# Performance work log

Measured on AMD Instinct MI355X. Metric: run time of the kernel, lower is better.

## Reference

```python
import jax, jax.numpy as jnp
import numpy as np

HID = 64  # GRU hidden size fixed in source: layers.GRU(64, ...)


def setup_inputs() -> dict:
    key = jax.random.key(0)
    ks = jax.random.split(key, 9)
    B, T, D, K = 128, 1024, 128, 32
    s = 0.05
    X = jax.random.normal(ks[0], (B, T, D), jnp.float32)
    mask = jnp.ones((B, T), jnp.int32)  # 1 = valid token
    # Keras GRU (reset_after=True) params
    gru_kernel = jax.random.normal(ks[1], (D, 3 * HID), jnp.float32) * s
    gru_rec_kernel = jax.random.normal(ks[2], (HID, 3 * HID), jnp.float32) * s
    gru_bias = jax.random.normal(ks[3], (2, 3 * HID), jnp.float32) * s  # [input_bias, recurrent_bias]
    # tfa.layers.CRF params: dense projection + chain kernel + boundary energies
    dense_kernel = jax.random.normal(ks[4], (HID, K), jnp.float32) * s
    dense_bias = jax.random.normal(ks[5], (K,), jnp.float32) * s
    chain_kernel = jax.random.normal(ks[6], (K, K), jnp.float32) * s
    left_boundary = jax.random.normal(ks[7], (K,), jnp.float32) * s
    right_boundary = jax.random.normal(ks[8], (K,), jnp.float32) * s
    return {"X": X, "mask": mask, "gru_kernel": gru_kernel,
            "gru_rec_kernel": gru_rec_kernel, "gru_bias": gru_bias,
            "dense_kernel": dense_kernel, "dense_bias": dense_bias,
            "chain_kernel": chain_kernel, "left_boundary": left_boundary,
            "right_boundary": right_boundary}


def gru_forward(X, mask_bool, gru_kernel, gru_rec_kernel, gru_bias):
    # Keras GRU, reset_after=True: z/r/h gate ordering, tanh/sigmoid activations.
    B, T, D = X.shape
    xproj = X @ gru_kernel + gru_bias[0]  # [B,T,3H] input projection (fused GEMM)

    def step(h, inp):
        xp, mt = inp  # xp: [B,3H], mt: [B] bool
        rec = h @ gru_rec_kernel + gru_bias[1]  # [B,3H]
        xz, xr, xh = jnp.split(xp, 3, axis=-1)
        rz, rr, rh = jnp.split(rec, 3, axis=-1)
        z = jax.nn.sigmoid(xz + rz)
        r = jax.nn.sigmoid(xr + rr)
        hh = jnp.tanh(xh + r * rh)
        hn = z * h + (1.0 - z) * hh
        hn = jnp.where(mt[:, None], hn, h)  # masked steps carry state
        return hn, hn

    h0 = jnp.zeros((B, HID), X.dtype)
    _, hs = jax.lax.scan(step, h0, (jnp.swapaxes(xproj, 0, 1), jnp.swapaxes(mask_bool, 0, 1)))
    return jnp.swapaxes(hs, 0, 1)  # [B,T,H]


def viterbi_decode(potentials, chain_kernel):
    # Max-plus DP with backpointers; potentials: [B,T,K]
    pots = jnp.swapaxes(potentials, 0, 1)  # [T,B,K]

    def fwd(score, pot_t):
        s = score[:, :, None] + chain_kernel[None]  # [B,K_from,K_to]
        bp = jnp.argmax(s, axis=1).astype(jnp.int32)  # [B,K]
        new_score = jnp.max(s, axis=1) + pot_t
        return new_score, bp

    final_score, bps = jax.lax.scan(fwd, pots[0], pots[1:])  # bps: [T-1,B,K]
    last_tag = jnp.argmax(final_score, axis=-1).astype(jnp.int32)  # [B]

    def back(tag, bp):
        prev = jnp.take_along_axis(bp, tag[:, None], axis=1)[:, 0]
        return prev, tag

    first_tag, tags = jax.lax.scan(back, last_tag, bps, reverse=True)  # tags[t] = tag at step t+1
    decoded = jnp.concatenate([first_tag[None], tags], axis=0)  # [T,B]
    return jnp.swapaxes(decoded, 0, 1)  # [B,T]


def reference(X, mask, gru_kernel, gru_rec_kernel, gru_bias,
              dense_kernel, dense_bias, chain_kernel,
              left_boundary, right_boundary):
    B, T, D = X.shape
    mask_bool = mask == 1
    hidden = gru_forward(X, mask_bool, gru_kernel, gru_rec_kernel, gru_bias)
    potentials = hidden @ dense_kernel + dense_bias  # [B,T,K] emissions
    seq_len = jnp.sum(mask, axis=1).astype(jnp.int32)  # [B]
    # Boundary energies (tfa CRF use_boundary=True): left at t=0, right at last valid step
    potentials = potentials.at[:, 0].add(left_boundary)
    potentials = potentials.at[jnp.arange(B), seq_len - 1].add(right_boundary)
    decoded = viterbi_decode(potentials, chain_kernel)  # [B,T] int32
    return decoded, potentials, seq_len, chain_kernel
```

## Files before the change

kernel.cpp:

```cpp
#include <hip/hip_runtime.h>
#include <math.h>

#define BB 128
#define TT 1024
#define DD 128
#define HH 64
#define G3 192
#define KK 32
#define CH 32

#define BCAST(v, l) __int_as_float(__builtin_amdgcn_readlane(__float_as_int(v), (l)))

__device__ int g_pflags[BB * 32];

__global__ __launch_bounds__(256, 2) void xproj_kernel(const float* __restrict__ X,
                                                       const float* __restrict__ Wk,
                                                       const float* __restrict__ gbias,
                                                       float* __restrict__ xp) {
    __shared__ float Xs[64 * 132];
    __shared__ float Ws[128 * 68];
    const int tid = threadIdx.x;
    const int row0 = blockIdx.x * 64;
    const int cg = blockIdx.y;
#pragma unroll
    for (int it = 0; it < 8; ++it) {
        int idx = it * 1024 + tid * 4;
        int r = idx >> 7, c = idx & 127;
        float4 v = *(const float4*)&X[((size_t)(row0 + r)) * DD + c];
        *(float4*)&Xs[r * 132 + c] = v;
    }
#pragma unroll
    for (int it = 0; it < 8; ++it) {
        int idx = it * 1024 + tid * 4;
        int k = idx >> 6, c = idx & 63;
        float4 v = *(const float4*)&Wk[(size_t)k * G3 + cg * 64 + c];
        *(float4*)&Ws[k * 68 + c] = v;
    }
    __syncthreads();
    const int tr = tid >> 4, tc = tid & 15;
    const int r0 = tr * 4, c0 = tc * 4;
    float acc[4][4];
#pragma unroll
    for (int r = 0; r < 4; ++r)
#pragma unroll
        for (int c = 0; c < 4; ++c) acc[r][c] = 0.f;
#pragma unroll 4
    for (int k = 0; k < DD; k += 4) {
        float a[4][4];
#pragma unroll
        for (int r = 0; r < 4; ++r) {
            float4 t = *(const float4*)&Xs[(r0 + r) * 132 + k];
            a[r][0] = t.x; a[r][1] = t.y; a[r][2] = t.z; a[r][3] = t.w;
        }
#pragma unroll
        for (int kk = 0; kk < 4; ++kk) {
            float4 b = *(const float4*)&Ws[(k + kk) * 68 + c0];
#pragma unroll
            for (int r = 0; r < 4; ++r) {
                acc[r][0] += a[r][kk] * b.x;
                acc[r][1] += a[r][kk] * b.y;
                acc[r][2] += a[r][kk] * b.z;
                acc[r][3] += a[r][kk] * b.w;
            }
        }
    }
    float4 bias = *(const float4*)&gbias[cg * 64 + c0];
#pragma unroll
    for (int r = 0; r < 4; ++r) {
        float4 o;
        o.x = acc[r][0] + bias.x; o.y = acc[r][1] + bias.y;
        o.z = acc[r][2] + bias.z; o.w = acc[r][3] + bias.w;
        *(float4*)&xp[((size_t)(row0 + r0 + r)) * G3 + cg * 64 + c0] = o;
    }
}

__global__ __launch_bounds__(256, 1)
void gruvit_kernel(const float* __restrict__ xp,
                   const float* __restrict__ Wr,
                   const float* __restrict__ gbias,
                   const int* __restrict__ mask,
                   const float* __restrict__ Dk,
                   const float* __restrict__ db,
                   const float* __restrict__ chain,
                   const float* __restrict__ lb,
                   const float* __restrict__ rb,
                   float* __restrict__ out_pot,
                   float* __restrict__ out_dec,
                   float* __restrict__ out_slen,
                   float* __restrict__ out_chn) {
    __shared__ __align__(16) unsigned char smem[73856];
    const int tid = threadIdx.x;
    const int w = tid >> 6;
    const int l = tid & 63;

    if (blockIdx.x < BB) {
        const int b = blockIdx.x;
        const int bTT = b * TT;
        float (*gbuf)[4 * HH]     = (float (*)[4 * HH])(smem);
        float (*hbuf)[HH]         = (float (*)[HH])(smem + 2048);
        float (*potring)[KK]      = (float (*)[KK])(smem + 3072);
        float (*xpstage)[CH * G3] = (float (*)[CH * G3])(smem + 11264);
        int (*maskst)[CH]         = (int (*)[CH])(smem + 60416);

        if (w < 3) {
            const int j = l;
            float wg[HH];
#pragma unroll
            for (int i2 = 0; i2 < HH; ++i2) wg[i2] = Wr[i2 * G3 + w * HH + j];
#pragma unroll
            for (int i2 = 0; i2 < HH; ++i2) asm volatile("" : "+v"(wg[i2]));
            const float bw = gbias[G3 + w * HH + j];
            __builtin_amdgcn_s_setprio(1);
            float h = 0.f;
            __syncthreads();
            float xv0 = xpstage[0][tid];
            int m0 = maskst[0][0];
            for (int i = 0; i < TT + 2; ++i) {
                if (i < TT) {
                    float a0 = bw, a1 = 0.f, a2 = 0.f, a3 = 0.f;
#pragma unroll
                    for (int c = 0; c < HH; c += 4) {
                        a0 += BCAST(h, c + 0) * wg[c + 0];
                        a1 += BCAST(h, c + 1) * wg[c + 1];
                        a2 += BCAST(h, c + 2) * wg[c + 2];
                        a3 += BCAST(h, c + 3) * wg[c + 3];
                    }
                    float a = (a0 + a1) + (a2 + a3);
                    float g = (w == 2) ? a : 1.f / (1.f + __expf(-(xv0 + a)));
                    gbuf[i & 1][w * HH + j] = g;
                    if (w == 2) gbuf[i & 1][3 * HH + j] = xv0;
                }
                __syncthreads();
                if (i < TT) {
                    float z  = gbuf[i & 1][j];
                    float r  = gbuf[i & 1][HH + j];
                    float rh = gbuf[i & 1][2 * HH + j];
                    float xh = gbuf[i & 1][3 * HH + j];
                    float y = xh + r * rh;
                    float hh = 1.f - 2.f / (1.f + __expf(2.f * y));
                    float hn = z * h + (1.f - z) * hh;
                    hn = (m0 != 0) ? hn : h;
                    h = hn;
                    if (w == 0) hbuf[i & 3][j] = hn;
                    if (i < TT - 1) {
                        const int t1 = i + 1;
                        xv0 = xpstage[(t1 >> 5) & 1][(t1 & 31) * G3 + tid];
                        m0  = maskst[(t1 >> 5) & 1][t1 & 31];
                    }
                }
            }
        } else {
            const int k = l & 31;
            int sl = 0;
#pragma unroll
            for (int q = 0; q < 16; ++q) sl += mask[bTT + q * 64 + l];
#pragma unroll
            for (int d = 32; d >= 1; d >>= 1) sl += __shfl_xor(sl, d, 64);
            if (l == 0) out_slen[b] = (float)sl;
            float dk[HH];
#pragma unroll
            for (int i2 = 0; i2 < HH; ++i2) dk[i2] = Dk[i2 * KK + k];
#pragma unroll
            for (int i2 = 0; i2 < HH; ++i2) asm volatile("" : "+v"(dk[i2]));
            const float dbk = db[k], lbk = lb[k], rbk = rb[k];
            const float* xpg = xp + (size_t)bTT * G3;
            float* potg = out_pot + (size_t)bTT * KK;
#pragma unroll
            for (int q = 0; q < 24; ++q) {
                float4 v = *(const float4*)&xpg[q * 256 + l * 4];
                *(float4*)&xpstage[0][q * 256 + l * 4] = v;
            }
            if (l < CH) maskst[0][l] = mask[bTT + l];
            __syncthreads();
            for (int i = 0; i < TT + 2; ++i) {
                if ((i & 31) == 0) {
                    const int cn = (i >> 5) + 1;
                    if (cn < 32) {
                        const float* src = xpg + (size_t)cn * CH * G3;
                        float* dst = &xpstage[cn & 1][0];
#pragma unroll
                        for (int q = 0; q < 24; ++q) {
                            float4 v = *(const float4*)&src[q * 256 + l * 4];
                            *(float4*)&dst[q * 256 + l * 4] = v;
                        }
                        if (l < CH) maskst[cn & 1][l] = mask[bTT + cn * CH + l];
                    }
                    const int cf = (i >> 5) - 2;
                    if (cf >= 0) {
                        const float* srcl = &potring[(cf & 1) * 32][0];
                        float* dstg = potg + (size_t)cf * CH * KK;
#pragma unroll
                        for (int q = 0; q < 4; ++q) {
                            float4 v = *(const float4*)&srcl[q * 256 + l * 4];
                            *(float4*)&dstg[q * 256 + l * 4] = v;
                        }
                    }
                }
                if ((i & 31) == 4 && l == 0) {
                    const int cp = (i >> 5) - 2;
                    if (cp >= 0) {
                        __threadfence();
                        atomicExch(&g_pflags[b * 32 + cp], 1);
                    }
                }
                const int t = i - 2;
                if (t >= 0 && t < TT) {
                    const float4* hv4 = (const float4*)&hbuf[t & 3][0];
                    float p0 = dbk, p1 = 0.f, p2 = 0.f, p3 = 0.f;
#pragma unroll
                    for (int c = 0; c < 16; ++c) {
                        float4 hv = hv4[c];
                        p0 += hv.x * dk[4 * c + 0];
                        p1 += hv.y * dk[4 * c + 1];
                        p2 += hv.z * dk[4 * c + 2];
                        p3 += hv.w * dk[4 * c + 3];
                    }
                    float pot = (p0 + p1) + (p2 + p3);
                    if (t == 0) pot += lbk;
                    if (t == sl - 1) pot += rbk;
                    if (l < 32) potring[t & 63][k] = pot;
                }
                __syncthreads();
            }
            {
                const float* srcl = &potring[(31 & 1) * 32][0];
                float* dstg = potg + (size_t)31 * CH * KK;
#pragma unroll
                for (int q = 0; q < 4; ++q) {
                    float4 v = *(const float4*)&srcl[q * 256 + l * 4];
                    *(float4*)&dstg[q * 256 + l * 4] = v;
                }
                if (l == 0) {
                    __threadfence();
                    atomicExch(&g_pflags[b * 32 + 30], 1);
                    atomicExch(&g_pflags[b * 32 + 31], 1);
                }
            }
        }
        return;
    }

    const int b = blockIdx.x - BB;
    const int bTT = b * TT;
    const float* potg = out_pot + (size_t)bTT * KK;
    const int k = l & 31;
    const int hf = l >> 5;
    const int addrx = (l ^ 32) * 4;

    unsigned char* bp    = smem;
    unsigned char* table = smem + 32736;
    float (*potbuf)[CH][KK] = (float (*)[CH][KK])(smem + 65504);
    int* ent        = (int*)(smem + 73696);
    int* last_tag_s = (int*)(smem + 73824);

    float ccol[16];
    int addr[16];
    if (w == 1) {
#pragma unroll
        for (int m = 0; m < 16; ++m) {
            ccol[m] = chain[(hf * 16 + m) * KK + k];
            addr[m] = (hf * 16 + m) * 4;
        }
#pragma unroll
        for (int m = 0; m < 16; ++m) asm volatile("" : "+v"(ccol[m]));
    }
    if (w == 0) {
        if (l == 0) {
            while (atomicAdd(&g_pflags[b * 32 + 0], 0) == 0) __builtin_amdgcn_s_sleep(8);
        }
        __threadfence();
#pragma unroll
        for (int q = 0; q < 4; ++q) {
            float4 v = *(const float4*)&potg[(size_t)(q * 64 + l) * 4];
            ((float4*)&potbuf[0][0][0])[q * 64 + l] = v;
        }
    }
    __syncthreads();
    float s = 0.f;
    for (int c = 0; c < 32; ++c) {
        if (w == 0 && c + 1 < 32) {
            if (l == 0) {
                while (atomicAdd(&g_pflags[b * 32 + c + 1], 0) == 0)
                    __builtin_amdgcn_s_sleep(8);
            }
            __threadfence();
            const float* src = potg + (size_t)(c + 1) * CH * KK;
#pragma unroll
            for (int q = 0; q < 4; ++q) {
                float4 v = *(const float4*)&src[(size_t)(q * 64 + l) * 4];
                ((float4*)&potbuf[(c + 1) & 1][0][0])[q * 64 + l] = v;
            }
        }
        if (w == 1) {
            for (int ll = 0; ll < 32; ++ll) {
                const int t = c * 32 + ll;
                float pot = potbuf[c & 1][ll][k];
                if (t == 0) {
                    s = pot;
                } else {
                    const int si = __float_as_int(s);
                    float cc[16];
#pragma unroll
                    for (int m = 0; m < 16; ++m)
                        cc[m] = __int_as_float(__builtin_amdgcn_ds_bpermute(addr[m], si)) + ccol[m];
                    float v1[8]; int i1[8];
#pragma unroll
                    for (int p = 0; p < 8; ++p) {
                        bool tk = cc[2 * p + 1] > cc[2 * p];
                        v1[p] = tk ? cc[2 * p + 1] : cc[2 * p];
                        i1[p] = hf * 16 + (tk ? 2 * p + 1 : 2 * p);
                    }
                    float v2[4]; int i2[4];
#pragma unroll
                    for (int p = 0; p < 4; ++p) {
                        bool tk = v1[2 * p + 1] > v1[2 * p];
                        v2[p] = tk ? v1[2 * p + 1] : v1[2 * p];
                        i2[p] = tk ? i1[2 * p + 1] : i1[2 * p];
                    }
                    float v3[2]; int i3[2];
#pragma unroll
                    for (int p = 0; p < 2; ++p) {
                        bool tk = v2[2 * p + 1] > v2[2 * p];
                        v3[p] = tk ? v2[2 * p + 1] : v2[2 * p];
                        i3[p] = tk ? i2[2 * p + 1] : i2[2 * p];
                    }
                    bool tk = v3[1] > v3[0];
                    float bv = tk ? v3[1] : v3[0];
                    int bi = tk ? i3[1] : i3[0];
                    float ov = __int_as_float(__builtin_amdgcn_ds_bpermute(addrx, __float_as_int(bv)));
                    int   oi = __builtin_amdgcn_ds_bpermute(addrx, bi);
                    bool take = (ov > bv) || (ov == bv && oi < bi);
                    if (take) { bv = ov; bi = oi; }
                    if (l < 32) bp[(t - 1) * KK + k] = (unsigned char)bi;
                    s = bv + pot;
                }
            }
        }
        __syncthreads();
    }
    if (w == 1) {
        float bv = s; int bi = k;
#pragma unroll
        for (int d = 16; d >= 1; d >>= 1) {
            float ov = __shfl_xor(bv, d, 64);
            int   oi = __shfl_xor(bi, d, 64);
            bool take = (ov > bv) || (ov == bv && oi < bi);
            if (take) { bv = ov; bi = oi; }
        }
        if (l == 0) *last_tag_s = bi;
    }
    __syncthreads();
    {
        const int kk2 = tid & 31;
        const int grp = tid >> 5;
        for (int c = grp; c < 32; c += 8) {
            int tag = kk2;
            for (int ll = 31; ll >= 0; --ll) {
                const int t = c * 32 + ll;
                if (t < TT - 1) tag = bp[t * KK + tag];
                table[(c * 32 + ll) * KK + kk2] = (unsigned char)tag;
            }
        }
    }
    __syncthreads();
    if (tid == 0) {
        int e = *last_tag_s;
        ent[31] = e;
        for (int c = 30; c >= 0; --c) { e = table[(c + 1) * 32 * KK + e]; ent[c] = e; }
    }
    __syncthreads();
    for (int t = tid; t < TT; t += 256) {
        const int c = t >> 5, ll = t & 31;
        out_dec[(size_t)bTT + t] = (float)table[(c * 32 + ll) * KK + ent[c]];
    }
    if (blockIdx.x == BB) {
        for (int i2 = tid; i2 < KK * KK; i2 += 256) out_chn[i2] = chain[i2];
    }
    for (int i2 = tid; i2 < 32; i2 += 256) atomicExch(&g_pflags[b * 32 + i2], 0);
}

extern "C" void kernel_launch(void* const* d_in, const int* in_sizes, int n_in,
                              void* d_out, int out_size, void* d_ws, size_t ws_size,
                              hipStream_t stream) {
    const float* X     = (const float*)d_in[0];
    const int*   mask  = (const int*)d_in[1];
    const float* Wk    = (const float*)d_in[2];
    const float* Wr    = (const float*)d_in[3];
    const float* gb    = (const float*)d_in[4];
    const float* Dk    = (const float*)d_in[5];
    const float* db    = (const float*)d_in[6];
    const float* chain = (const float*)d_in[7];
    const float* lb    = (const float*)d_in[8];
    const float* rb    = (const float*)d_in[9];

    float* out = (float*)d_out;
    float* out_dec  = out;
    float* out_pot  = out + (size_t)BB * TT;
    float* out_slen = out + (size_t)BB * TT + (size_t)BB * TT * KK;
    float* out_chn  = out_slen + BB;

    float* xp = (float*)d_ws;

    xproj_kernel<<<dim3((BB * TT) / 64, 3), dim3(256), 0, stream>>>(X, Wk, gb, xp);
    gruvit_kernel<<<dim3(2 * BB), dim3(256), 0, stream>>>(xp, Wr, gb, mask, Dk, db,
                                                          chain, lb, rb, out_pot,
                                                          out_dec, out_slen, out_chn);
}
```

Baseline: 745.9 us.

## Fuse GRU input projection GEMM into the per-batch recurrent kernel prologue

Removes the separate xproj kernel launch. Each of the 128 recurrent blocks now computes its own sequence's input projection in a prologue, holding the whole input weight matrix in enlarged shared memory, before the serial GRU scan starts. This saves a launch and the global-wide GEMM phase. In exchange the GEMM runs on only 128 blocks instead of thousands, adds a serial prologue before each recurrence, and raises shared memory use, which limits occupancy.

```diff
diff --git a/kernel.cpp b/kernel.cpp
--- a/kernel.cpp
+++ b/kernel.cpp
@@ -13,69 +13,10 @@
 
 __device__ int g_pflags[BB * 32];
 
-__global__ __launch_bounds__(256, 2) void xproj_kernel(const float* __restrict__ X,
-                                                       const float* __restrict__ Wk,
-                                                       const float* __restrict__ gbias,
-                                                       float* __restrict__ xp) {
-    __shared__ float Xs[64 * 132];
-    __shared__ float Ws[128 * 68];
-    const int tid = threadIdx.x;
-    const int row0 = blockIdx.x * 64;
-    const int cg = blockIdx.y;
-#pragma unroll
-    for (int it = 0; it < 8; ++it) {
-        int idx = it * 1024 + tid * 4;
-        int r = idx >> 7, c = idx & 127;
-        float4 v = *(const float4*)&X[((size_t)(row0 + r)) * DD + c];
-        *(float4*)&Xs[r * 132 + c] = v;
-    }
-#pragma unroll
-    for (int it = 0; it < 8; ++it) {
-        int idx = it * 1024 + tid * 4;
-        int k = idx >> 6, c = idx & 63;
-        float4 v = *(const float4*)&Wk[(size_t)k * G3 + cg * 64 + c];
-        *(float4*)&Ws[k * 68 + c] = v;
-    }
-    __syncthreads();
-    const int tr = tid >> 4, tc = tid & 15;
-    const int r0 = tr * 4, c0 = tc * 4;
-    float acc[4][4];
-#pragma unroll
-    for (int r = 0; r < 4; ++r)
-#pragma unroll
-        for (int c = 0; c < 4; ++c) acc[r][c] = 0.f;
-#pragma unroll 4
-    for (int k = 0; k < DD; k += 4) {
-        float a[4][4];
-#pragma unroll
-        for (int r = 0; r < 4; ++r) {
-            float4 t = *(const float4*)&Xs[(r0 + r) * 132 + k];
-            a[r][0] = t.x; a[r][1] = t.y; a[r][2] = t.z; a[r][3] = t.w;
-        }
-#pragma unroll
-        for (int kk = 0; kk < 4; ++kk) {
-            float4 b = *(const float4*)&Ws[(k + kk) * 68 + c0];
-#pragma unroll
-            for (int r = 0; r < 4; ++r) {
-                acc[r][0] += a[r][kk] * b.x;
-                acc[r][1] += a[r][kk] * b.y;
-                acc[r][2] += a[r][kk] * b.z;
-                acc[r][3] += a[r][kk] * b.w;
-            }
-        }
-    }
-    float4 bias = *(const float4*)&gbias[cg * 64 + c0];
-#pragma unroll
-    for (int r = 0; r < 4; ++r) {
-        float4 o;
-        o.x = acc[r][0] + bias.x; o.y = acc[r][1] + bias.y;
-        o.z = acc[r][2] + bias.z; o.w = acc[r][3] + bias.w;
-        *(float4*)&xp[((size_t)(row0 + r0 + r)) * G3 + cg * 64 + c0] = o;
-    }
-}
-
 __global__ __launch_bounds__(256, 1)
-void gruvit_kernel(const float* __restrict__ xp,
+void gruvit_kernel(const float* __restrict__ X,
+                   const float* __restrict__ Wk,
+                   const float* __restrict__ xp,
                    const float* __restrict__ Wr,
                    const float* __restrict__ gbias,
                    const int* __restrict__ mask,
@@ -88,7 +29,7 @@
                    float* __restrict__ out_dec,
                    float* __restrict__ out_slen,
                    float* __restrict__ out_chn) {
-    __shared__ __align__(16) unsigned char smem[73856];
+    __shared__ __align__(16) unsigned char smem[134144];
     const int tid = threadIdx.x;
     const int w = tid >> 6;
     const int l = tid & 63;
@@ -96,6 +37,69 @@
     if (blockIdx.x < BB) {
         const int b = blockIdx.x;
         const int bTT = b * TT;
+
+        {
+            float* Xs = (float*)smem;
+            float* Ws = (float*)(smem + 33792);
+#pragma unroll
+            for (int it = 0; it < 24; ++it) {
+                int idx = it * 256 + tid;
+                int kr = idx / 48, cc = (idx % 48) * 4;
+                float4 v = *(const float4*)&Wk[(size_t)kr * G3 + cc];
+                *(float4*)&Ws[kr * 196 + cc] = v;
+            }
+            const int tr = tid >> 4, tc = tid & 15;
+            const int r0 = tr * 4, c0 = tc * 4;
+            float* xpw = (float*)xp + (size_t)bTT * G3;
+            for (int rt = 0; rt < 16; ++rt) {
+                const int row0 = rt * 64;
+#pragma unroll
+                for (int it = 0; it < 8; ++it) {
+                    int idx = it * 256 + tid;
+                    int r = idx >> 5, c4 = (idx & 31) << 2;
+                    float4 v = *(const float4*)&X[((size_t)(bTT + row0 + r)) * DD + c4];
+                    *(float4*)&Xs[r * 132 + c4] = v;
+                }
+                __syncthreads();
+                for (int cg = 0; cg < 3; ++cg) {
+                    float acc[4][4];
+#pragma unroll
+                    for (int r = 0; r < 4; ++r)
+#pragma unroll
+                        for (int c = 0; c < 4; ++c) acc[r][c] = 0.f;
+#pragma unroll 4
+                    for (int k2 = 0; k2 < DD; k2 += 4) {
+                        float a[4][4];
+#pragma unroll
+                        for (int r = 0; r < 4; ++r) {
+                            float4 t = *(const float4*)&Xs[(r0 + r) * 132 + k2];
+                            a[r][0] = t.x; a[r][1] = t.y; a[r][2] = t.z; a[r][3] = t.w;
+                        }
+#pragma unroll
+                        for (int kk = 0; kk < 4; ++kk) {
+                            float4 bv = *(const float4*)&Ws[(k2 + kk) * 196 + cg * 64 + c0];
+#pragma unroll
+                            for (int r = 0; r < 4; ++r) {
+                                acc[r][0] += a[r][kk] * bv.x;
+                                acc[r][1] += a[r][kk] * bv.y;
+                                acc[r][2] += a[r][kk] * bv.z;
+                                acc[r][3] += a[r][kk] * bv.w;
+                            }
+                        }
+                    }
+                    float4 bias = *(const float4*)&gbias[cg * 64 + c0];
+#pragma unroll
+                    for (int r = 0; r < 4; ++r) {
+                        float4 o;
+                        o.x = acc[r][0] + bias.x; o.y = acc[r][1] + bias.y;
+                        o.z = acc[r][2] + bias.z; o.w = acc[r][3] + bias.w;
+                        *(float4*)&xpw[((size_t)(row0 + r0 + r)) * G3 + cg * 64 + c0] = o;
+                    }
+                }
+                __syncthreads();
+            }
+        }
+
         float (*gbuf)[4 * HH]     = (float (*)[4 * HH])(smem);
         float (*hbuf)[HH]         = (float (*)[HH])(smem + 2048);
         float (*potring)[KK]      = (float (*)[KK])(smem + 3072);
@@ -401,8 +405,8 @@
 
     float* xp = (float*)d_ws;
 
-    xproj_kernel<<<dim3((BB * TT) / 64, 3), dim3(256), 0, stream>>>(X, Wk, gb, xp);
-    gruvit_kernel<<<dim3(2 * BB), dim3(256), 0, stream>>>(xp, Wr, gb, mask, Dk, db,
-                                                          chain, lb, rb, out_pot,
-                                                          out_dec, out_slen, out_chn);
+    gruvit_kernel<<<dim3(2 * BB), dim3(256), 0, stream>>>(X, Wk, xp, Wr, gb, mask,
+                                                          Dk, db, chain, lb, rb,
+                                                          out_pot, out_dec,
+                                                          out_slen, out_chn);
 }
```

Result: slower. 880.4 us (+18.0%).

## Move emission projection from GRU block into Viterbi block via hidden-state handoff

Applied to the files above, without the earlier changes.

The GRU blocks no longer stage xproj chunks through shared memory or compute the dense emission projection. Each GRU wave now loads its xproj values straight from global memory with a two-step register prefetch, and wave 3 writes the hidden state into the consumed xproj buffer. The Viterbi block reads those hidden states per chunk, computes potentials itself and writes them out. This shortens the serial GRU critical path by removing the staging, the second barrier per step and the projection work, at the cost of global-latency loads inside the recurrence and more work on the Viterbi side.

```diff
diff --git a/kernel.cpp b/kernel.cpp
--- a/kernel.cpp
+++ b/kernel.cpp
@@ -88,7 +88,7 @@
                    float* __restrict__ out_dec,
                    float* __restrict__ out_slen,
                    float* __restrict__ out_chn) {
-    __shared__ __align__(16) unsigned char smem[73856];
+    __shared__ __align__(16) unsigned char smem[82048];
     const int tid = threadIdx.x;
     const int w = tid >> 6;
     const int l = tid & 63;
@@ -96,14 +96,11 @@
     if (blockIdx.x < BB) {
         const int b = blockIdx.x;
         const int bTT = b * TT;
-        float (*gbuf)[4 * HH]     = (float (*)[4 * HH])(smem);
-        float (*hbuf)[HH]         = (float (*)[HH])(smem + 2048);
-        float (*potring)[KK]      = (float (*)[KK])(smem + 3072);
-        float (*xpstage)[CH * G3] = (float (*)[CH * G3])(smem + 11264);
-        int (*maskst)[CH]         = (int (*)[CH])(smem + 60416);
+        float (*gbuf)[4 * HH] = (float (*)[4 * HH])(smem);
+        const float* xpg = xp + (size_t)bTT * G3;
+        const int j = l;
 
         if (w < 3) {
-            const int j = l;
             float wg[HH];
 #pragma unroll
             for (int i2 = 0; i2 < HH; ++i2) wg[i2] = Wr[i2 * G3 + w * HH + j];
@@ -112,129 +109,67 @@
             const float bw = gbias[G3 + w * HH + j];
             __builtin_amdgcn_s_setprio(1);
             float h = 0.f;
-            __syncthreads();
-            float xv0 = xpstage[0][tid];
-            int m0 = maskst[0][0];
-            for (int i = 0; i < TT + 2; ++i) {
-                if (i < TT) {
-                    float a0 = bw, a1 = 0.f, a2 = 0.f, a3 = 0.f;
-#pragma unroll
-                    for (int c = 0; c < HH; c += 4) {
-                        a0 += BCAST(h, c + 0) * wg[c + 0];
-                        a1 += BCAST(h, c + 1) * wg[c + 1];
-                        a2 += BCAST(h, c + 2) * wg[c + 2];
-                        a3 += BCAST(h, c + 3) * wg[c + 3];
-                    }
-                    float a = (a0 + a1) + (a2 + a3);
-                    float g = (w == 2) ? a : 1.f / (1.f + __expf(-(xv0 + a)));
-                    gbuf[i & 1][w * HH + j] = g;
-                    if (w == 2) gbuf[i & 1][3 * HH + j] = xv0;
-                }
+            float xv_c = xpg[w * HH + j];
+            float xv_n = xpg[(size_t)G3 + w * HH + j];
+            int m_c = mask[bTT], m_n = mask[bTT + 1];
+            for (int t = 0; t < TT; ++t) {
+                float xv_n2 = 0.f; int m_n2 = 0;
+                if (t + 2 < TT) {
+                    xv_n2 = xpg[(size_t)(t + 2) * G3 + w * HH + j];
+                    m_n2  = mask[bTT + t + 2];
+                }
+                float a0 = bw, a1 = 0.f, a2 = 0.f, a3 = 0.f;
+#pragma unroll
+                for (int c = 0; c < HH; c += 4) {
+                    a0 += BCAST(h, c + 0) * wg[c + 0];
+                    a1 += BCAST(h, c + 1) * wg[c + 1];
+                    a2 += BCAST(h, c + 2) * wg[c + 2];
+                    a3 += BCAST(h, c + 3) * wg[c + 3];
+                }
+                float a = (a0 + a1) + (a2 + a3);
+                float g = (w == 2) ? a : 1.f / (1.f + __expf(-(xv_c + a)));
+                gbuf[t & 1][w * HH + j] = g;
+                if (w == 2) gbuf[t & 1][3 * HH + j] = xv_c;
                 __syncthreads();
-                if (i < TT) {
-                    float z  = gbuf[i & 1][j];
-                    float r  = gbuf[i & 1][HH + j];
-                    float rh = gbuf[i & 1][2 * HH + j];
-                    float xh = gbuf[i & 1][3 * HH + j];
-                    float y = xh + r * rh;
-                    float hh = 1.f - 2.f / (1.f + __expf(2.f * y));
-                    float hn = z * h + (1.f - z) * hh;
-                    hn = (m0 != 0) ? hn : h;
-                    h = hn;
-                    if (w == 0) hbuf[i & 3][j] = hn;
-                    if (i < TT - 1) {
-                        const int t1 = i + 1;
-                        xv0 = xpstage[(t1 >> 5) & 1][(t1 & 31) * G3 + tid];
-                        m0  = maskst[(t1 >> 5) & 1][t1 & 31];
-                    }
-                }
+                float z  = gbuf[t & 1][j];
+                float r  = gbuf[t & 1][HH + j];
+                float rh = gbuf[t & 1][2 * HH + j];
+                float xh = gbuf[t & 1][3 * HH + j];
+                float y = xh + r * rh;
+                float hh = 1.f - 2.f / (1.f + __expf(2.f * y));
+                float hn = z * h + (1.f - z) * hh;
+                h = (m_c != 0) ? hn : h;
+                xv_c = xv_n; xv_n = xv_n2; m_c = m_n; m_n = m_n2;
             }
         } else {
-            const int k = l & 31;
-            int sl = 0;
-#pragma unroll
-            for (int q = 0; q < 16; ++q) sl += mask[bTT + q * 64 + l];
-#pragma unroll
-            for (int d = 32; d >= 1; d >>= 1) sl += __shfl_xor(sl, d, 64);
-            if (l == 0) out_slen[b] = (float)sl;
-            float dk[HH];
-#pragma unroll
-            for (int i2 = 0; i2 < HH; ++i2) dk[i2] = Dk[i2 * KK + k];
-#pragma unroll
-            for (int i2 = 0; i2 < HH; ++i2) asm volatile("" : "+v"(dk[i2]));
-            const float dbk = db[k], lbk = lb[k], rbk = rb[k];
-            const float* xpg = xp + (size_t)bTT * G3;
-            float* potg = out_pot + (size_t)bTT * KK;
-#pragma unroll
-            for (int q = 0; q < 24; ++q) {
-                float4 v = *(const float4*)&xpg[q * 256 + l * 4];
-                *(float4*)&xpstage[0][q * 256 + l * 4] = v;
-            }
-            if (l < CH) maskst[0][l] = mask[bTT + l];
-            __syncthreads();
-            for (int i = 0; i < TT + 2; ++i) {
-                if ((i & 31) == 0) {
-                    const int cn = (i >> 5) + 1;
-                    if (cn < 32) {
-                        const float* src = xpg + (size_t)cn * CH * G3;
-                        float* dst = &xpstage[cn & 1][0];
-#pragma unroll
-                        for (int q = 0; q < 24; ++q) {
-                            float4 v = *(const float4*)&src[q * 256 + l * 4];
-                            *(float4*)&dst[q * 256 + l * 4] = v;
-                        }
-                        if (l < CH) maskst[cn & 1][l] = mask[bTT + cn * CH + l];
-                    }
-                    const int cf = (i >> 5) - 2;
-                    if (cf >= 0) {
-                        const float* srcl = &potring[(cf & 1) * 32][0];
-                        float* dstg = potg + (size_t)cf * CH * KK;
-#pragma unroll
-                        for (int q = 0; q < 4; ++q) {
-                            float4 v = *(const float4*)&srcl[q * 256 + l * 4];
-                            *(float4*)&dstg[q * 256 + l * 4] = v;
-                        }
-                    }
-                }
-                if ((i & 31) == 4 && l == 0) {
-                    const int cp = (i >> 5) - 2;
-                    if (cp >= 0) {
+            float h = 0.f;
+            int m_c = mask[bTT], m_n = mask[bTT + 1];
+            float* hout = (float*)xp + (size_t)bTT * G3;
+            for (int t = 0; t < TT; ++t) {
+                int m_n2 = 0;
+                if (t + 2 < TT) m_n2 = mask[bTT + t + 2];
+                __syncthreads();
+                float z  = gbuf[t & 1][j];
+                float r  = gbuf[t & 1][HH + j];
+                float rh = gbuf[t & 1][2 * HH + j];
+                float xh = gbuf[t & 1][3 * HH + j];
+                float y = xh + r * rh;
+                float hh = 1.f - 2.f / (1.f + __expf(2.f * y));
+                float hn = z * h + (1.f - z) * hh;
+                h = (m_c != 0) ? hn : h;
+                hout[(size_t)t * G3 + j] = h;
+                if ((t & 31) == 4) {
+                    const int cp = (t >> 5) - 1;
+                    if (cp >= 0 && l == 0) {
                         __threadfence();
                         atomicExch(&g_pflags[b * 32 + cp], 1);
                     }
                 }
-                const int t = i - 2;
-                if (t >= 0 && t < TT) {
-                    const float4* hv4 = (const float4*)&hbuf[t & 3][0];
-                    float p0 = dbk, p1 = 0.f, p2 = 0.f, p3 = 0.f;
-#pragma unroll
-                    for (int c = 0; c < 16; ++c) {
-                        float4 hv = hv4[c];
-                        p0 += hv.x * dk[4 * c + 0];
-                        p1 += hv.y * dk[4 * c + 1];
-                        p2 += hv.z * dk[4 * c + 2];
-                        p3 += hv.w * dk[4 * c + 3];
-                    }
-                    float pot = (p0 + p1) + (p2 + p3);
-                    if (t == 0) pot += lbk;
-                    if (t == sl - 1) pot += rbk;
-                    if (l < 32) potring[t & 63][k] = pot;
-                }
-                __syncthreads();
-            }
-            {
-                const float* srcl = &potring[(31 & 1) * 32][0];
-                float* dstg = potg + (size_t)31 * CH * KK;
-#pragma unroll
-                for (int q = 0; q < 4; ++q) {
-                    float4 v = *(const float4*)&srcl[q * 256 + l * 4];
-                    *(float4*)&dstg[q * 256 + l * 4] = v;
-                }
-                if (l == 0) {
-                    __threadfence();
-                    atomicExch(&g_pflags[b * 32 + 30], 1);
-                    atomicExch(&g_pflags[b * 32 + 31], 1);
-                }
+                m_c = m_n; m_n = m_n2;
+            }
+            if (l == 0) {
+                __threadfence();
+                atomicExch(&g_pflags[b * 32 + 31], 1);
             }
         }
         return;
@@ -242,7 +177,8 @@
 
     const int b = blockIdx.x - BB;
     const int bTT = b * TT;
-    const float* potg = out_pot + (size_t)bTT * KK;
+    const float* hsrc = xp + (size_t)bTT * G3;
+    float* potg = out_pot + (size_t)bTT * KK;
     const int k = l & 31;
     const int hf = l >> 5;
     const int addrx = (l ^ 32) * 4;
@@ -250,8 +186,9 @@
     unsigned char* bp    = smem;
     unsigned char* table = smem + 32736;
     float (*potbuf)[CH][KK] = (float (*)[CH][KK])(smem + 65504);
-    int* ent        = (int*)(smem + 73696);
-    int* last_tag_s = (int*)(smem + 73824);
+    float (*hstage)[HH]     = (float (*)[HH])(smem + 73696);
+    int* ent        = (int*)(smem + 81888);
+    int* last_tag_s = (int*)(smem + 82016);
 
     float ccol[16];
     int addr[16];
@@ -264,31 +201,84 @@
 #pragma unroll
         for (int m = 0; m < 16; ++m) asm volatile("" : "+v"(ccol[m]));
     }
+    float dk[HH];
+    float dbk = 0.f, lbk = 0.f, rbk = 0.f;
+    int sl = 0;
     if (w == 0) {
+#pragma unroll
+        for (int q = 0; q < 16; ++q) sl += mask[bTT + q * 64 + l];
+#pragma unroll
+        for (int d = 32; d >= 1; d >>= 1) sl += __shfl_xor(sl, d, 64);
+        if (l == 0) out_slen[b] = (float)sl;
+#pragma unroll
+        for (int i2 = 0; i2 < HH; ++i2) dk[i2] = Dk[i2 * KK + k];
+#pragma unroll
+        for (int i2 = 0; i2 < HH; ++i2) asm volatile("" : "+v"(dk[i2]));
+        dbk = db[k]; lbk = lb[k]; rbk = rb[k];
         if (l == 0) {
             while (atomicAdd(&g_pflags[b * 32 + 0], 0) == 0) __builtin_amdgcn_s_sleep(8);
         }
         __threadfence();
 #pragma unroll
-        for (int q = 0; q < 4; ++q) {
-            float4 v = *(const float4*)&potg[(size_t)(q * 64 + l) * 4];
-            ((float4*)&potbuf[0][0][0])[q * 64 + l] = v;
+        for (int q = 0; q < 8; ++q) {
+            const int idx = q * 64 + l, r = idx >> 4, c4 = idx & 15;
+            float4 v = *(const float4*)&hsrc[(size_t)r * G3 + c4 * 4];
+            *(float4*)&hstage[r][c4 * 4] = v;
+        }
+        for (int r = 0; r < 32; ++r) {
+            const float4* hv4 = (const float4*)&hstage[r][0];
+            float p0 = dbk, p1 = 0.f, p2 = 0.f, p3 = 0.f;
+#pragma unroll
+            for (int c = 0; c < 16; ++c) {
+                float4 hv = hv4[c];
+                p0 += hv.x * dk[4 * c + 0];
+                p1 += hv.y * dk[4 * c + 1];
+                p2 += hv.z * dk[4 * c + 2];
+                p3 += hv.w * dk[4 * c + 3];
+            }
+            float pot = (p0 + p1) + (p2 + p3);
+            if (r == 0) pot += lbk;
+            if (r == sl - 1) pot += rbk;
+            if (l < 32) {
+                potbuf[0][r][k] = pot;
+                potg[(size_t)r * KK + k] = pot;
+            }
         }
     }
     __syncthreads();
     float s = 0.f;
     for (int c = 0; c < 32; ++c) {
         if (w == 0 && c + 1 < 32) {
+            const int cc = c + 1;
             if (l == 0) {
-                while (atomicAdd(&g_pflags[b * 32 + c + 1], 0) == 0)
+                while (atomicAdd(&g_pflags[b * 32 + cc], 0) == 0)
                     __builtin_amdgcn_s_sleep(8);
             }
             __threadfence();
-            const float* src = potg + (size_t)(c + 1) * CH * KK;
-#pragma unroll
-            for (int q = 0; q < 4; ++q) {
-                float4 v = *(const float4*)&src[(size_t)(q * 64 + l) * 4];
-                ((float4*)&potbuf[(c + 1) & 1][0][0])[q * 64 + l] = v;
+#pragma unroll
+            for (int q = 0; q < 8; ++q) {
+                const int idx = q * 64 + l, r = idx >> 4, c4 = idx & 15;
+                float4 v = *(const float4*)&hsrc[(size_t)(cc * 32 + r) * G3 + c4 * 4];
+                *(float4*)&hstage[r][c4 * 4] = v;
+            }
+            for (int r = 0; r < 32; ++r) {
+                const float4* hv4 = (const float4*)&hstage[r][0];
+                float p0 = dbk, p1 = 0.f, p2 = 0.f, p3 = 0.f;
+#pragma unroll
+                for (int cc2 = 0; cc2 < 16; ++cc2) {
+                    float4 hv = hv4[cc2];
+                    p0 += hv.x * dk[4 * cc2 + 0];
+                    p1 += hv.y * dk[4 * cc2 + 1];
+                    p2 += hv.z * dk[4 * cc2 + 2];
+                    p3 += hv.w * dk[4 * cc2 + 3];
+                }
+                float pot = (p0 + p1) + (p2 + p3);
+                const int t = cc * 32 + r;
+                if (t == sl - 1) pot += rbk;
+                if (l < 32) {
+                    potbuf[cc & 1][r][k] = pot;
+                    potg[(size_t)t * KK + k] = pot;
+                }
             }
         }
         if (w == 1) {
```

Result: no change. 742.9 us (-0.4%).
